# Optimization experiments

Measured on AMD Instinct MI355X. Metric: run time of the kernel, lower is better.

The kernel has to match this reference:

```python
import jax, jax.numpy as jnp
import numpy as np

# grid derived from output_shape=[1,10,200,176,128]: sparse_shape = (10+1, 200, 176)
D, H, W = 11, 200, 176
C_IN = 128
C_MID = 64
NUM_VOX = 16000
BN_EPS = 1e-5
DN = ('NCDHW', 'OIDHW', 'NCDHW')


def conv3d(x, w, stride, padding):
    return jax.lax.conv_general_dilated(x, w, window_strides=stride,
                                        padding=padding, dimension_numbers=DN)


def setup_inputs() -> dict:
    key = jax.random.key(0)
    ks = jax.random.split(key, 12)
    voxel_features = jax.random.normal(ks[0], (NUM_VOX, C_IN), dtype=jnp.float32)
    # unique active voxel coords (batch, z, y, x)
    lin = jax.random.choice(ks[1], D * H * W, (NUM_VOX,), replace=False)
    z = lin // (H * W)
    r = lin % (H * W)
    y = r // W
    x = r % W
    b = jnp.zeros((NUM_VOX,), dtype=jnp.int32)
    coors = jnp.stack([b, z.astype(jnp.int32), y.astype(jnp.int32), x.astype(jnp.int32)], axis=1)
    s = 0.05
    w1 = jax.random.normal(ks[2], (C_MID, C_IN, 3, 3, 3), jnp.float32) * s   # subm0
    w2 = jax.random.normal(ks[3], (C_MID, C_MID, 3, 1, 1), jnp.float32) * s  # strided
    w3 = jax.random.normal(ks[4], (C_MID, C_MID, 3, 3, 3), jnp.float32) * s  # subm1
    w4 = jax.random.normal(ks[5], (C_MID, C_MID, 3, 3, 3), jnp.float32) * s  # subm1
    w5 = jax.random.normal(ks[6], (C_MID, C_MID, 3, 1, 1), jnp.float32) * s  # strided
    bn_gamma = 1.0 + 0.1 * jax.random.normal(ks[7], (5, C_MID), jnp.float32)
    bn_beta = 0.1 * jax.random.normal(ks[8], (5, C_MID), jnp.float32)
    bn_mean = 0.1 * jax.random.normal(ks[9], (5, C_MID), jnp.float32)
    bn_var = 1.0 + 0.1 * jax.random.uniform(ks[10], (5, C_MID), jnp.float32)
    return {"voxel_features": voxel_features, "w1": w1, "w2": w2, "w3": w3,
            "w4": w4, "w5": w5, "bn_gamma": bn_gamma, "bn_beta": bn_beta,
            "bn_mean": bn_mean, "bn_var": bn_var, "coors": coors, "batch_size": 1}


def _bn_relu(x, i, mask, bn_gamma, bn_beta, bn_mean, bn_var):
    # inference-mode BatchNorm1d over active voxels (mask keeps inactive sites at 0)
    scale = (bn_gamma[i] / jnp.sqrt(bn_var[i] + BN_EPS))[None, :, None, None, None]
    shift = (bn_beta[i] - bn_mean[i] * bn_gamma[i] / jnp.sqrt(bn_var[i] + BN_EPS))[None, :, None, None, None]
    return jnp.maximum(x * scale + shift, 0.0) * mask


def reference(voxel_features, w1, w2, w3, w4, w5, bn_gamma, bn_beta, bn_mean, bn_var, coors, batch_size):
    N = int(batch_size)
    b, z, y, x = coors[:, 0], coors[:, 1], coors[:, 2], coors[:, 3]
    dense = jnp.zeros((N, C_IN, D, H, W), voxel_features.dtype).at[b, :, z, y, x].set(voxel_features)
    mask = jnp.zeros((N, 1, D, H, W), voxel_features.dtype).at[b, :, z, y, x].set(1.0)
    ones_k = jnp.ones((1, 1, 3, 1, 1), voxel_features.dtype)

    # SubMConv3d(128->64, k3, pad1): dense conv then restrict to active input sites
    h = conv3d(dense, w1, (1, 1, 1), [(1, 1), (1, 1), (1, 1)]) * mask
    h = _bn_relu(h, 0, mask, bn_gamma, bn_beta, bn_mean, bn_var)

    # SparseConv3d(64->64, k=(3,1,1), s=(2,1,1), pad0): new active set
    h = conv3d(h, w2, (2, 1, 1), 'VALID')
    mask = (conv3d(mask, ones_k, (2, 1, 1), 'VALID') > 0).astype(h.dtype)
    h = _bn_relu(h, 1, mask, bn_gamma, bn_beta, bn_mean, bn_var)

    # SubMConv3d(64->64) x2
    h = conv3d(h, w3, (1, 1, 1), [(1, 1), (1, 1), (1, 1)]) * mask
    h = _bn_relu(h, 2, mask, bn_gamma, bn_beta, bn_mean, bn_var)
    h = conv3d(h, w4, (1, 1, 1), [(1, 1), (1, 1), (1, 1)]) * mask
    h = _bn_relu(h, 3, mask, bn_gamma, bn_beta, bn_mean, bn_var)

    # SparseConv3d(64->64, (3,1,1), (2,1,1))
    h = conv3d(h, w5, (2, 1, 1), 'VALID')
    mask = (conv3d(mask, ones_k, (2, 1, 1), 'VALID') > 0).astype(h.dtype)
    h = _bn_relu(h, 4, mask, bn_gamma, bn_beta, bn_mean, bn_var)

    n, c, d, hh, ww = h.shape  # (1, 64, 2, 200, 176)
    return h.reshape(n, c * d, hh, ww)
```

## Files before the change

kernel.cpp:

```cpp
#include <hip/hip_runtime.h>

constexpr int D0  = 11;
constexpr int Hh  = 200;
constexpr int Ww  = 176;
constexpr int HWC = Hh * Ww;
constexpr int NV  = 16000;
constexpr int ND1 = 5;
constexpr int ND2 = 2;
constexpr int CAPN = 32000;
constexpr float EPS = 1e-5f;

#define PC(i) ((i) << 5)

__device__ inline int wave_append(bool has, int* counter) {
    unsigned long long m = __ballot(has);
    if (!m) return -1;
    int lane = threadIdx.x & 63;
    int leader = __builtin_ctzll(m);
    int base = 0;
    if (lane == leader) base = atomicAdd(counter, (int)__popcll(m));
    base = __shfl(base, leader);
    return has ? base + (int)__popcll(m & ((1ull << lane) - 1)) : -1;
}

__device__ inline int block_append(bool has, int* counter, int* lds) {
    int tid = threadIdx.x;
    int w = tid >> 6, lane = tid & 63;
    unsigned long long m = __ballot(has);
    if (lane == 0) lds[w] = (int)__popcll(m);
    __syncthreads();
    if (tid == 0) {
        int t0 = lds[0], t1 = lds[1], t2 = lds[2], t3 = lds[3];
        int base = atomicAdd(counter, t0 + t1 + t2 + t3);
        lds[4] = base;
        lds[5] = base + t0;
        lds[6] = base + t0 + t1;
        lds[7] = base + t0 + t1 + t2;
    }
    __syncthreads();
    int base = lds[4 + w];
    return has ? base + (int)__popcll(m & ((1ull << lane) - 1)) : -1;
}

__global__ __launch_bounds__(256) void setup1_k(const int* __restrict__ coors,
    int* __restrict__ grid0,
    const float* __restrict__ w1, const float* __restrict__ w2,
    const float* __restrict__ w3, const float* __restrict__ w4,
    const float* __restrict__ w5,
    float* __restrict__ w1t, float* __restrict__ w2t, float* __restrict__ w3t,
    float* __restrict__ w4t, float* __restrict__ w5t) {
    int idx = blockIdx.x * 256 + threadIdx.x;
    int role = blockIdx.y;
    if (role == 0) {
        if (idx < NV) {
            int4 c = reinterpret_cast<const int4*>(coors)[idx];
            grid0[c.y * HWC + c.z * Ww + c.w] = idx;
        }
        return;
    }
    const float* src; float* dst; int I, K;
    switch (role) {
        case 1:  src = w1; dst = w1t; I = 128; K = 27; break;
        case 2:  src = w2; dst = w2t; I = 64;  K = 3;  break;
        case 3:  src = w3; dst = w3t; I = 64;  K = 27; break;
        case 4:  src = w4; dst = w4t; I = 64;  K = 27; break;
        default: src = w5; dst = w5t; I = 64;  K = 3;  break;
    }
    int tot = 64 * I * K;
    if (idx >= tot) return;
    int o = idx / (I * K), r = idx % (I * K), ii = r / K, k = r % K;
    dst[(k * I + ii) * 64 + o] = src[idx];
}

__global__ __launch_bounds__(256) void setup2_k(const int* __restrict__ coors,
    const int* __restrict__ grid0, int* __restrict__ grid1,
    int* __restrict__ list1, int* __restrict__ list2, int* __restrict__ ctr,
    int2* __restrict__ pairs1) {
    __shared__ int lds[8];
    int bid = blockIdx.x, tid = threadIdx.x;
    if (bid < 688) {
        int p = bid * 256 + tid;
        bool occ = false;
        if (p < ND1 * HWC) {
            int d1 = p / HWC, yx = p - d1 * HWC;
            int b = (2 * d1) * HWC + yx;
            occ = (grid0[b] >= 0) || (grid0[b + HWC] >= 0) || (grid0[b + 2 * HWC] >= 0);
        }
        int s = block_append(occ, ctr + PC(0), lds);
        if (occ) { grid1[p] = s; list1[s] = p; }
    } else if (bid < 963) {
        int p = (bid - 688) * 256 + tid;
        bool occ = false;
        if (p < ND2 * HWC) {
            int d2 = p / HWC, yx = p - d2 * HWC;
            #pragma unroll
            for (int dd = 0; dd < 7; ++dd) occ |= (grid0[(4 * d2 + dd) * HWC + yx] >= 0);
        }
        int s = block_append(occ, ctr + PC(1), lds);
        if (occ) list2[s] = p;
    } else {
        int idx = (bid - 963) * 256 + tid;
        int k = idx / NV;
        bool has = false; int j = -1;
        int i = idx - k * NV;
        if (idx < 27 * NV) {
            int4 c = reinterpret_cast<const int4*>(coors)[i];
            int kd = k / 9, r = k % 9, kh = r / 3, kw = r % 3;
            int zz = c.y + kd - 1, yy = c.z + kh - 1, xx = c.w + kw - 1;
            if ((unsigned)zz < (unsigned)D0 && (unsigned)yy < (unsigned)Hh &&
                (unsigned)xx < (unsigned)Ww) {
                j = grid0[zz * HWC + yy * Ww + xx];
                has = j >= 0;
            }
        }
        int rel = wave_append(has, ctr + PC(2 + k));
        if (has) { int2 pr; pr.x = j; pr.y = i; pairs1[k * NV + rel] = pr; }
    }
}

__global__ __launch_bounds__(256) void setup3_k(const int* __restrict__ grid0,
    const int* __restrict__ grid1, const int* __restrict__ list1,
    const int* __restrict__ list2, int* __restrict__ ctr,
    int2* __restrict__ pairs2, int2* __restrict__ pairs34,
    int2* __restrict__ pairs5) {
    int bid = blockIdx.x, tid = threadIdx.x;
    int n1 = ctr[PC(0)], n2 = ctr[PC(1)];
    if (bid < 375) {
        int idx = bid * 256 + tid;
        int k = idx / CAPN;
        int s1 = idx - k * CAPN;
        bool has = false; int j = -1;
        if (s1 < n1) {
            int p = list1[s1]; int d1 = p / HWC, yx = p - d1 * HWC;
            j = grid0[(2 * d1 + k) * HWC + yx];
            has = j >= 0;
        }
        int rel = wave_append(has, ctr + PC(29 + k));
        if (has) { int2 pr; pr.x = j; pr.y = s1; pairs2[k * CAPN + rel] = pr; }
    } else if (bid < 3750) {
        int idx = (bid - 375) * 256 + tid;
        int k = idx / CAPN;
        int s1 = idx - k * CAPN;
        bool has = false; int j = -1;
        if (s1 < n1) {
            int p = list1[s1];
            int d1 = p / HWC, yx = p - d1 * HWC, y = yx / Ww, x = yx - y * Ww;
            int kd = k / 9, r = k % 9, kh = r / 3, kw = r % 3;
            int dd = d1 + kd - 1, yy = y + kh - 1, xx = x + kw - 1;
            if ((unsigned)dd < (unsigned)ND1 && (unsigned)yy < (unsigned)Hh &&
                (unsigned)xx < (unsigned)Ww) {
                j = grid1[dd * HWC + yy * Ww + xx];
                has = j >= 0;
            }
        }
        int rel = wave_append(has, ctr + PC(32 + k));
        if (has) { int2 pr; pr.x = j; pr.y = s1; pairs34[k * CAPN + rel] = pr; }
    } else {
        int idx = (bid - 3750) * 256 + tid;
        int k = idx / CAPN;
        int s2 = idx - k * CAPN;
        bool has = false; int j = -1;
        if (s2 < n2) {
            int p = list2[s2]; int d2 = p / HWC, yx = p - d2 * HWC;
            j = grid1[(2 * d2 + k) * HWC + yx];
            has = j >= 0;
        }
        int rel = wave_append(has, ctr + PC(59 + k));
        if (has) { int2 pr; pr.x = j; pr.y = s2; pairs5[k * CAPN + rel] = pr; }
    }
}

template<int XS, bool HALF, int NT, int STRIDE>
__global__ __launch_bounds__(256, 4) void pconv_k(
    const float* __restrict__ fin, const float* __restrict__ wt,
    const int2* __restrict__ pairs, const int* __restrict__ cnt,
    float* __restrict__ acc) {
    const int lane = threadIdx.x & 63;
    const int wid = __builtin_amdgcn_readfirstlane(
        (int)blockIdx.x * 4 + ((int)threadIdx.x >> 6));
    const int nw = (int)gridDim.x * 4;

    int sum = 0;
    #pragma unroll
    for (int k = 0; k < NT; ++k) sum += cnt[k << 5];
    const int total = HALF ? 2 * sum : sum;

    int chunk = (total + nw - 1) / nw;
    int v = wid * chunk;
    int v1 = v + chunk; if (v1 > total) v1 = total;
    if (v >= v1) return;

    int s = 0, soff_s = 0;
    int send = cnt[0];
    while (v >= send) { soff_s = send; ++s; send += cnt[(HALF ? (s >> 1) : s) << 5]; }

    float w[64];
    int xofs = 0;
    const int2* pb = nullptr;
    bool need = true;
    while (v < v1) {
        while (v >= send) { soff_s = send; ++s; send += cnt[(HALF ? (s >> 1) : s) << 5]; need = true; }
        if (need) {
            const float* wp = wt + (size_t)s * 4096 + lane;
            #pragma unroll
            for (int c = 0; c < 64; ++c) w[c] = wp[(size_t)c * 64];
            if (HALF) xofs = (s & 1) * 64;
            pb = pairs + (size_t)(HALF ? (s >> 1) : s) * STRIDE - soff_s;
            need = false;
        }
        int e = v1 < send ? v1 : send;
        for (; v + 1 < e; v += 2) {
            int2 prA = pb[v];
            int2 prB = pb[v + 1];
            int ja = __builtin_amdgcn_readfirstlane(prA.x);
            int ya = __builtin_amdgcn_readfirstlane(prA.y);
            int jb = __builtin_amdgcn_readfirstlane(prB.x);
            int yb = __builtin_amdgcn_readfirstlane(prB.y);
            const float* xa = fin + (size_t)ja * XS + xofs;
            const float* xb = fin + (size_t)jb * XS + xofs;
            float a0=0.f,a1=0.f,a2=0.f,a3=0.f,b0=0.f,b1=0.f,b2=0.f,b3=0.f;
            #pragma unroll
            for (int c = 0; c < 64; c += 4) {
                a0 = fmaf(xa[c],     w[c],     a0);
                a1 = fmaf(xa[c + 1], w[c + 1], a1);
                a2 = fmaf(xa[c + 2], w[c + 2], a2);
                a3 = fmaf(xa[c + 3], w[c + 3], a3);
                b0 = fmaf(xb[c],     w[c],     b0);
                b1 = fmaf(xb[c + 1], w[c + 1], b1);
                b2 = fmaf(xb[c + 2], w[c + 2], b2);
                b3 = fmaf(xb[c + 3], w[c + 3], b3);
            }
            unsafeAtomicAdd(acc + ((size_t)ya << 6) + lane, (a0 + a1) + (a2 + a3));
            unsafeAtomicAdd(acc + ((size_t)yb << 6) + lane, (b0 + b1) + (b2 + b3));
        }
        if (v < e) {
            int2 pr = pb[v]; ++v;
            int jp = __builtin_amdgcn_readfirstlane(pr.x);
            int yp = __builtin_amdgcn_readfirstlane(pr.y);
            const float* xp = fin + (size_t)jp * XS + xofs;
            float a0=0.f,a1=0.f,a2=0.f,a3=0.f;
            #pragma unroll
            for (int c = 0; c < 64; c += 4) {
                a0 = fmaf(xp[c],     w[c],     a0);
                a1 = fmaf(xp[c + 1], w[c + 1], a1);
                a2 = fmaf(xp[c + 2], w[c + 2], a2);
                a3 = fmaf(xp[c + 3], w[c + 3], a3);
            }
            unsafeAtomicAdd(acc + ((size_t)yp << 6) + lane, (a0 + a1) + (a2 + a3));
        }
    }
}

template<bool ZERO, bool FIXEDN>
__global__ __launch_bounds__(256) void bn_k(float* __restrict__ acc,
    float* __restrict__ f, const int* __restrict__ ctr,
    const float* __restrict__ bg, const float* __restrict__ bb,
    const float* __restrict__ bm, const float* __restrict__ bv) {
    int idx = blockIdx.x * 256 + threadIdx.x;
    int site = idx >> 6, o = idx & 63;
    int n = FIXEDN ? NV : ctr[PC(0)];
    if (site < n) {
        float sc = bg[o] / sqrtf(bv[o] + EPS);
        float sh = bb[o] - bm[o] * sc;
        f[idx] = fmaxf(fmaf(acc[idx], sc, sh), 0.f);
        if (ZERO) acc[idx] = 0.f;
    }
}

__global__ __launch_bounds__(256) void bn5_k(const float* __restrict__ acc5,
    const int* __restrict__ list2, const int* __restrict__ ctr,
    const float* __restrict__ bg, const float* __restrict__ bb,
    const float* __restrict__ bm, const float* __restrict__ bv,
    float* __restrict__ out) {
    __shared__ float tile[64 * 65];
    __shared__ int pp[64];
    int n2 = ctr[PC(1)];
    int sb = blockIdx.x * 64;
    int tid = threadIdx.x;
    if (tid < 64) pp[tid] = (sb + tid < n2) ? list2[sb + tid] : -1;
    int o = tid & 63;
    float sc = bg[o] / sqrtf(bv[o] + EPS);
    float sh = bb[o] - bm[o] * sc;
    __syncthreads();
    #pragma unroll
    for (int it = 0; it < 16; ++it) {
        int sl = it * 4 + (tid >> 6);
        int s2 = sb + sl;
        if (s2 < n2)
            tile[sl * 65 + o] = fmaxf(fmaf(acc5[(size_t)s2 * 64 + o], sc, sh), 0.f);
    }
    __syncthreads();
    #pragma unroll
    for (int it = 0; it < 16; ++it) {
        int og = it * 4 + (tid >> 6);
        int sl = tid & 63;
        int p = pp[sl];
        if (p >= 0) {
            int d2 = p / HWC, yx = p - d2 * HWC;
            out[(size_t)(og * ND2 + d2) * HWC + yx] = tile[sl * 65 + og];
        }
    }
}

extern "C" void kernel_launch(void* const* d_in, const int* in_sizes, int n_in,
                              void* d_out, int out_size, void* d_ws, size_t ws_size,
                              hipStream_t stream) {
    const float* vf = (const float*)d_in[0];
    const float* w1 = (const float*)d_in[1];
    const float* w2 = (const float*)d_in[2];
    const float* w3 = (const float*)d_in[3];
    const float* w4 = (const float*)d_in[4];
    const float* w5 = (const float*)d_in[5];
    const float* bg = (const float*)d_in[6];
    const float* bb = (const float*)d_in[7];
    const float* bm = (const float*)d_in[8];
    const float* bv = (const float*)d_in[9];
    const int* coors = (const int*)d_in[10];
    float* out = (float*)d_out;

    char* ws = (char*)d_ws;
    size_t off = 0;
    auto take = [&](size_t n) -> void* {
        void* pp = ws + off;
        off += (n + 255) & ~(size_t)255;
        return pp;
    };
    int*   ctr  = (int*)take(16384);
    float* acc1 = (float*)take((size_t)NV * 64 * 4);
    float* accX = (float*)take((size_t)CAPN * 64 * 4);
    float* acc5 = (float*)take((size_t)CAPN * 64 * 4);
    size_t zero_len = (char*)acc5 + (size_t)CAPN * 64 * 4 - (char*)ctr;
    int*   grid0 = (int*)take((size_t)D0 * HWC * 4);
    int*   grid1 = (int*)take((size_t)ND1 * HWC * 4);
    size_t ff_len = (char*)grid1 + (size_t)ND1 * HWC * 4 - (char*)grid0;
    int*   list1 = (int*)take(CAPN * 4);
    int*   list2 = (int*)take(CAPN * 4);
    float* w1t = (float*)take((size_t)27 * 128 * 64 * 4);
    float* w2t = (float*)take((size_t)3 * 64 * 64 * 4);
    float* w3t = (float*)take((size_t)27 * 64 * 64 * 4);
    float* w4t = (float*)take((size_t)27 * 64 * 64 * 4);
    float* w5t = (float*)take((size_t)3 * 64 * 64 * 4);
    float* fA  = (float*)take((size_t)NV * 64 * 4);
    float* fB  = (float*)take((size_t)CAPN * 64 * 4);
    int2*  pairs1  = (int2*)take((size_t)27 * NV * 8);
    int2*  pairs2  = (int2*)take((size_t)3 * CAPN * 8);
    int2*  pairs34 = (int2*)take((size_t)27 * CAPN * 8);
    int2*  pairs5  = (int2*)take((size_t)3 * CAPN * 8);

    hipMemsetAsync(ctr, 0x00, zero_len, stream);
    hipMemsetAsync(grid0, 0xFF, ff_len, stream);
    hipMemsetAsync(out, 0x00, (size_t)out_size * 4, stream);

    setup1_k<<<dim3(864, 6), 256, 0, stream>>>(coors, grid0, w1, w2, w3, w4, w5,
                                               w1t, w2t, w3t, w4t, w5t);
    setup2_k<<<2651, 256, 0, stream>>>(coors, grid0, grid1, list1, list2, ctr, pairs1);
    setup3_k<<<4125, 256, 0, stream>>>(grid0, grid1, list1, list2, ctr,
                                       pairs2, pairs34, pairs5);

    pconv_k<128, true, 27, NV><<<1024, 256, 0, stream>>>(vf, w1t, pairs1,
                                                         ctr + PC(2), acc1);
    bn_k<false, true><<<(NV * 64) / 256, 256, 0, stream>>>(acc1, fA, ctr,
        bg, bb, bm, bv);
    pconv_k<64, false, 3, CAPN><<<1024, 256, 0, stream>>>(fA, w2t, pairs2,
                                                          ctr + PC(29), accX);
    bn_k<true, false><<<(CAPN * 64) / 256, 256, 0, stream>>>(accX, fB, ctr,
        bg + 64, bb + 64, bm + 64, bv + 64);
    pconv_k<64, false, 27, CAPN><<<1024, 256, 0, stream>>>(fB, w3t, pairs34,
                                                           ctr + PC(32), accX);
    bn_k<true, false><<<(CAPN * 64) / 256, 256, 0, stream>>>(accX, fB, ctr,
        bg + 128, bb + 128, bm + 128, bv + 128);
    pconv_k<64, false, 27, CAPN><<<1024, 256, 0, stream>>>(fB, w4t, pairs34,
                                                           ctr + PC(32), accX);
    bn_k<false, false><<<(CAPN * 64) / 256, 256, 0, stream>>>(accX, fB, ctr,
        bg + 192, bb + 192, bm + 192, bv + 192);
    pconv_k<64, false, 3, CAPN><<<1024, 256, 0, stream>>>(fB, w5t, pairs5,
                                                          ctr + PC(59), acc5);
    bn5_k<<<CAPN / 64, 256, 0, stream>>>(acc5, list2, ctr,
        bg + 256, bb + 256, bm + 256, bv + 256, out);
}
```

Measured before the change: 248.9 us.

## Split pair-conv input channels across waves and write dense output directly

The gather-scatter convolution kernel now gives each wave a quarter (or an eighth for the 128-channel layer) of the input channels per offset. This cuts the per-wave weight registers from 64 to 16 and raises parallelism, and it replaces the old half-channel split scheme. The cost is more atomic accumulations into the output and repeated pair reads across waves. The final BN kernel now runs over every dense output site using a new grid2 index map, so it writes zeros itself and the separate output memset is removed.

```diff
diff --git a/kernel.cpp b/kernel.cpp
--- a/kernel.cpp
+++ b/kernel.cpp
@@ -73,7 +73,7 @@
 }
 
 __global__ __launch_bounds__(256) void setup2_k(const int* __restrict__ coors,
-    const int* __restrict__ grid0, int* __restrict__ grid1,
+    const int* __restrict__ grid0, int* __restrict__ grid1, int* __restrict__ grid2,
     int* __restrict__ list1, int* __restrict__ list2, int* __restrict__ ctr,
     int2* __restrict__ pairs1) {
     __shared__ int lds[8];
@@ -97,7 +97,7 @@
             for (int dd = 0; dd < 7; ++dd) occ |= (grid0[(4 * d2 + dd) * HWC + yx] >= 0);
         }
         int s = block_append(occ, ctr + PC(1), lds);
-        if (occ) list2[s] = p;
+        if (occ) { list2[s] = p; grid2[p] = s; }
     } else {
         int idx = (bid - 963) * 256 + tid;
         int k = idx / NV;
@@ -127,8 +127,7 @@
     int n1 = ctr[PC(0)], n2 = ctr[PC(1)];
     if (bid < 375) {
         int idx = bid * 256 + tid;
-        int k = idx / CAPN;
-        int s1 = idx - k * CAPN;
+        int k = idx / CAPN, s1 = idx - k * CAPN;
         bool has = false; int j = -1;
         if (s1 < n1) {
             int p = list1[s1]; int d1 = p / HWC, yx = p - d1 * HWC;
@@ -139,8 +138,7 @@
         if (has) { int2 pr; pr.x = j; pr.y = s1; pairs2[k * CAPN + rel] = pr; }
     } else if (bid < 3750) {
         int idx = (bid - 375) * 256 + tid;
-        int k = idx / CAPN;
-        int s1 = idx - k * CAPN;
+        int k = idx / CAPN, s1 = idx - k * CAPN;
         bool has = false; int j = -1;
         if (s1 < n1) {
             int p = list1[s1];
@@ -157,8 +155,7 @@
         if (has) { int2 pr; pr.x = j; pr.y = s1; pairs34[k * CAPN + rel] = pr; }
     } else {
         int idx = (bid - 3750) * 256 + tid;
-        int k = idx / CAPN;
-        int s2 = idx - k * CAPN;
+        int k = idx / CAPN, s2 = idx - k * CAPN;
         bool has = false; int j = -1;
         if (s2 < n2) {
             int p = list2[s2]; int d2 = p / HWC, yx = p - d2 * HWC;
@@ -170,7 +167,7 @@
     }
 }
 
-template<int XS, bool HALF, int NT, int STRIDE>
+template<int XS, int QN, int NT, int WS, int STRIDE>
 __global__ __launch_bounds__(256, 4) void pconv_k(
     const float* __restrict__ fin, const float* __restrict__ wt,
     const int2* __restrict__ pairs, const int* __restrict__ cnt,
@@ -179,33 +176,33 @@
     const int wid = __builtin_amdgcn_readfirstlane(
         (int)blockIdx.x * 4 + ((int)threadIdx.x >> 6));
     const int nw = (int)gridDim.x * 4;
-
-    int sum = 0;
+    const int qw  = wid & (QN - 1);
+    const int rid = wid / QN;
+    const int nr  = nw / QN;
+
+    int total = 0;
     #pragma unroll
-    for (int k = 0; k < NT; ++k) sum += cnt[k << 5];
-    const int total = HALF ? 2 * sum : sum;
-
-    int chunk = (total + nw - 1) / nw;
-    int v = wid * chunk;
+    for (int k = 0; k < NT; ++k) total += cnt[k << 5];
+
+    int chunk = (total + nr - 1) / nr;
+    int v = rid * chunk;
     int v1 = v + chunk; if (v1 > total) v1 = total;
     if (v >= v1) return;
 
-    int s = 0, soff_s = 0;
+    int s = 0, soff = 0;
     int send = cnt[0];
-    while (v >= send) { soff_s = send; ++s; send += cnt[(HALF ? (s >> 1) : s) << 5]; }
-
-    float w[64];
-    int xofs = 0;
+    while (v >= send) { soff = send; ++s; send += cnt[s << 5]; }
+
+    float w[16];
     const int2* pb = nullptr;
     bool need = true;
     while (v < v1) {
-        while (v >= send) { soff_s = send; ++s; send += cnt[(HALF ? (s >> 1) : s) << 5]; need = true; }
+        while (v >= send) { soff = send; ++s; send += cnt[s << 5]; need = true; }
         if (need) {
-            const float* wp = wt + (size_t)s * 4096 + lane;
+            const float* wp = wt + (size_t)s * WS + qw * 1024 + lane;
             #pragma unroll
-            for (int c = 0; c < 64; ++c) w[c] = wp[(size_t)c * 64];
-            if (HALF) xofs = (s & 1) * 64;
-            pb = pairs + (size_t)(HALF ? (s >> 1) : s) * STRIDE - soff_s;
+            for (int c = 0; c < 16; ++c) w[c] = wp[(size_t)c * 64];
+            pb = pairs + (size_t)s * STRIDE - soff;
             need = false;
         }
         int e = v1 < send ? v1 : send;
@@ -216,11 +213,11 @@
             int ya = __builtin_amdgcn_readfirstlane(prA.y);
             int jb = __builtin_amdgcn_readfirstlane(prB.x);
             int yb = __builtin_amdgcn_readfirstlane(prB.y);
-            const float* xa = fin + (size_t)ja * XS + xofs;
-            const float* xb = fin + (size_t)jb * XS + xofs;
+            const float* xa = fin + (size_t)ja * XS + qw * 16;
+            const float* xb = fin + (size_t)jb * XS + qw * 16;
             float a0=0.f,a1=0.f,a2=0.f,a3=0.f,b0=0.f,b1=0.f,b2=0.f,b3=0.f;
             #pragma unroll
-            for (int c = 0; c < 64; c += 4) {
+            for (int c = 0; c < 16; c += 4) {
                 a0 = fmaf(xa[c],     w[c],     a0);
                 a1 = fmaf(xa[c + 1], w[c + 1], a1);
                 a2 = fmaf(xa[c + 2], w[c + 2], a2);
@@ -237,10 +234,10 @@
             int2 pr = pb[v]; ++v;
             int jp = __builtin_amdgcn_readfirstlane(pr.x);
             int yp = __builtin_amdgcn_readfirstlane(pr.y);
-            const float* xp = fin + (size_t)jp * XS + xofs;
+            const float* xp = fin + (size_t)jp * XS + qw * 16;
             float a0=0.f,a1=0.f,a2=0.f,a3=0.f;
             #pragma unroll
-            for (int c = 0; c < 64; c += 4) {
+            for (int c = 0; c < 16; c += 4) {
                 a0 = fmaf(xp[c],     w[c],     a0);
                 a1 = fmaf(xp[c + 1], w[c + 1], a1);
                 a2 = fmaf(xp[c + 2], w[c + 2], a2);
@@ -268,16 +265,15 @@
 }
 
 __global__ __launch_bounds__(256) void bn5_k(const float* __restrict__ acc5,
-    const int* __restrict__ list2, const int* __restrict__ ctr,
+    const int* __restrict__ grid2,
     const float* __restrict__ bg, const float* __restrict__ bb,
     const float* __restrict__ bm, const float* __restrict__ bv,
     float* __restrict__ out) {
     __shared__ float tile[64 * 65];
     __shared__ int pp[64];
-    int n2 = ctr[PC(1)];
     int sb = blockIdx.x * 64;
     int tid = threadIdx.x;
-    if (tid < 64) pp[tid] = (sb + tid < n2) ? list2[sb + tid] : -1;
+    if (tid < 64) pp[tid] = grid2[sb + tid];
     int o = tid & 63;
     float sc = bg[o] / sqrtf(bv[o] + EPS);
     float sh = bb[o] - bm[o] * sc;
@@ -285,20 +281,18 @@
     #pragma unroll
     for (int it = 0; it < 16; ++it) {
         int sl = it * 4 + (tid >> 6);
-        int s2 = sb + sl;
-        if (s2 < n2)
-            tile[sl * 65 + o] = fmaxf(fmaf(acc5[(size_t)s2 * 64 + o], sc, sh), 0.f);
+        int s2 = pp[sl];
+        tile[sl * 65 + o] = (s2 >= 0)
+            ? fmaxf(fmaf(acc5[(size_t)s2 * 64 + o], sc, sh), 0.f) : 0.f;
     }
     __syncthreads();
     #pragma unroll
     for (int it = 0; it < 16; ++it) {
         int og = it * 4 + (tid >> 6);
         int sl = tid & 63;
-        int p = pp[sl];
-        if (p >= 0) {
-            int d2 = p / HWC, yx = p - d2 * HWC;
-            out[(size_t)(og * ND2 + d2) * HWC + yx] = tile[sl * 65 + og];
-        }
+        int site = sb + sl;
+        int d2 = site / HWC, yx = site - d2 * HWC;
+        out[(size_t)(og * ND2 + d2) * HWC + yx] = tile[sl * 65 + og];
     }
 }
 
@@ -332,7 +326,8 @@
     size_t zero_len = (char*)acc5 + (size_t)CAPN * 64 * 4 - (char*)ctr;
     int*   grid0 = (int*)take((size_t)D0 * HWC * 4);
     int*   grid1 = (int*)take((size_t)ND1 * HWC * 4);
-    size_t ff_len = (char*)grid1 + (size_t)ND1 * HWC * 4 - (char*)grid0;
+    int*   grid2 = (int*)take((size_t)ND2 * HWC * 4);
+    size_t ff_len = (char*)grid2 + (size_t)ND2 * HWC * 4 - (char*)grid0;
     int*   list1 = (int*)take(CAPN * 4);
     int*   list2 = (int*)take(CAPN * 4);
     float* w1t = (float*)take((size_t)27 * 128 * 64 * 4);
@@ -349,32 +344,32 @@
 
     hipMemsetAsync(ctr, 0x00, zero_len, stream);
     hipMemsetAsync(grid0, 0xFF, ff_len, stream);
-    hipMemsetAsync(out, 0x00, (size_t)out_size * 4, stream);
 
     setup1_k<<<dim3(864, 6), 256, 0, stream>>>(coors, grid0, w1, w2, w3, w4, w5,
                                                w1t, w2t, w3t, w4t, w5t);
-    setup2_k<<<2651, 256, 0, stream>>>(coors, grid0, grid1, list1, list2, ctr, pairs1);
+    setup2_k<<<2651, 256, 0, stream>>>(coors, grid0, grid1, grid2,
+                                       list1, list2, ctr, pairs1);
     setup3_k<<<4125, 256, 0, stream>>>(grid0, grid1, list1, list2, ctr,
                                        pairs2, pairs34, pairs5);
 
-    pconv_k<128, true, 27, NV><<<1024, 256, 0, stream>>>(vf, w1t, pairs1,
-                                                         ctr + PC(2), acc1);
+    pconv_k<128, 8, 27, 8192, NV><<<1024, 256, 0, stream>>>(
+        vf, w1t, pairs1, ctr + PC(2), acc1);
     bn_k<false, true><<<(NV * 64) / 256, 256, 0, stream>>>(acc1, fA, ctr,
         bg, bb, bm, bv);
-    pconv_k<64, false, 3, CAPN><<<1024, 256, 0, stream>>>(fA, w2t, pairs2,
-                                                          ctr + PC(29), accX);
+    pconv_k<64, 4, 3, 4096, CAPN><<<1024, 256, 0, stream>>>(
+        fA, w2t, pairs2, ctr + PC(29), accX);
     bn_k<true, false><<<(CAPN * 64) / 256, 256, 0, stream>>>(accX, fB, ctr,
         bg + 64, bb + 64, bm + 64, bv + 64);
-    pconv_k<64, false, 27, CAPN><<<1024, 256, 0, stream>>>(fB, w3t, pairs34,
-                                                           ctr + PC(32), accX);
+    pconv_k<64, 4, 27, 4096, CAPN><<<1024, 256, 0, stream>>>(
+        fB, w3t, pairs34, ctr + PC(32), accX);
     bn_k<true, false><<<(CAPN * 64) / 256, 256, 0, stream>>>(accX, fB, ctr,
         bg + 128, bb + 128, bm + 128, bv + 128);
-    pconv_k<64, false, 27, CAPN><<<1024, 256, 0, stream>>>(fB, w4t, pairs34,
-                                                           ctr + PC(32), accX);
+    pconv_k<64, 4, 27, 4096, CAPN><<<1024, 256, 0, stream>>>(
+        fB, w4t, pairs34, ctr + PC(32), accX);
     bn_k<false, false><<<(CAPN * 64) / 256, 256, 0, stream>>>(accX, fB, ctr,
         bg + 192, bb + 192, bm + 192, bv + 192);
-    pconv_k<64, false, 3, CAPN><<<1024, 256, 0, stream>>>(fB, w5t, pairs5,
-                                                          ctr + PC(59), acc5);
-    bn5_k<<<CAPN / 64, 256, 0, stream>>>(acc5, list2, ctr,
+    pconv_k<64, 4, 3, 4096, CAPN><<<1024, 256, 0, stream>>>(
+        fB, w5t, pairs5, ctr + PC(59), acc5);
+    bn5_k<<<(ND2 * HWC) / 64, 256, 0, stream>>>(acc5, grid2,
         bg + 256, bb + 256, bm + 256, bv + 256, out);
 }
```

Result: slower. 435.5 us (+75.0%).
